# Kernel optimization log

Hardware: AMD Instinct MI355X
Metric: run time of the kernel (lower is better)

## Reference

```python
import jax, jax.numpy as jnp
import numpy as np

N_NODES = 100000


def gcn_conv(x, src, dst, W, b, n):
    # x: [N, F_in]; src/dst: [E+N] (self-loops already appended)
    h = x @ W  # [N, F_out]
    deg = jax.ops.segment_sum(jnp.ones_like(dst, dtype=h.dtype), dst, num_segments=n)
    dinv = jnp.where(deg > 0, jax.lax.rsqrt(deg), 0.0)
    norm = dinv[src] * dinv[dst]  # [E+N]
    msgs = h[src] * norm[:, None]  # gather + scale
    out = jax.ops.segment_sum(msgs, dst, num_segments=n)  # scatter-add at dst
    return out + b


def setup_inputs() -> dict:
    key = jax.random.key(0)
    k1, k2, k3, ke = jax.random.split(key, 4)
    d = 64
    x = jax.random.normal(k1, (N_NODES, d), dtype=jnp.float32)
    edge_index = jax.random.randint(ke, (2, 1000000), 0, N_NODES, dtype=jnp.int64)
    s = 1.0 / np.sqrt(d)
    W1 = jax.random.normal(k2, (d, d), dtype=jnp.float32) * s
    b1 = jnp.zeros((d,), dtype=jnp.float32)
    W2 = jax.random.normal(k3, (d, d), dtype=jnp.float32) * s
    b2 = jnp.zeros((d,), dtype=jnp.float32)
    return {"x": x, "edge_index": edge_index, "W1": W1, "b1": b1, "W2": W2, "b2": b2}


def reference(x, edge_index, W1, b1, W2, b2):
    n = x.shape[0]
    loops = jnp.arange(n, dtype=edge_index.dtype)
    src = jnp.concatenate([edge_index[0], loops])
    dst = jnp.concatenate([edge_index[1], loops])
    h = gcn_conv(x, src, dst, W1, b1, n)
    h = jax.nn.relu(h)
    out = gcn_conv(h, src, dst, W2, b2, n)
    return out
```

## Files before the change

### kernel.cpp

```cpp
#include <hip/hip_runtime.h>

#define F 64
#define NCH 64

typedef __attribute__((ext_vector_type(8))) short bf16x8;
typedef __attribute__((ext_vector_type(4))) float f32x4;

static __device__ __forceinline__ unsigned short f2bf(float f) {
    unsigned u = __float_as_uint(f);
    return (unsigned short)((u + 0x7fffu + ((u >> 16) & 1u)) >> 16);
}
static __device__ __forceinline__ float bflo(unsigned u) { return __uint_as_float(u << 16); }
static __device__ __forceinline__ float bfhi(unsigned u) { return __uint_as_float(u & 0xffff0000u); }

__global__ __launch_bounds__(256) void k_prep(const float* __restrict__ W1,
                                              const float* __restrict__ W2,
                                              unsigned short* __restrict__ W1t,
                                              unsigned short* __restrict__ W2t) {
    const float* W = blockIdx.x ? W2 : W1;
    unsigned short* Wt = blockIdx.x ? W2t : W1t;
    const int t = threadIdx.x;
#pragma unroll
    for (int i = 0; i < 16; ++i) {
        int e = t + i * 256;
        int n = e >> 6, k = e & 63;
        Wt[e] = f2bf(W[k * 64 + n]);
    }
}

__global__ __launch_bounds__(256) void k_hist(const int* __restrict__ dst,
                                              int* __restrict__ histM,
                                              int E, int chunk, int NB) {
    extern __shared__ int h[];
    const int t = threadIdx.x;
    for (int i = t; i < NB; i += 256) h[i] = 0;
    __syncthreads();
    const int lo = blockIdx.x * chunk;
    const int hi = min(E, lo + chunk);
    for (int e = lo + t; e < hi; e += 256) {
        atomicAdd(&h[dst[e] >> 8], 1);
    }
    __syncthreads();
    for (int i = t; i < NB; i += 256) histM[i * NCH + blockIdx.x] = h[i];
}

__global__ __launch_bounds__(256) void s_part(const int* __restrict__ v,
                                              int* __restrict__ part, int M) {
    __shared__ int sd[256];
    const int t = threadIdx.x;
    const int base = blockIdx.x * 1024 + t * 4;
    int4 d = *(const int4*)&v[base];
    sd[t] = d.x + d.y + d.z + d.w;
    __syncthreads();
    for (int off = 128; off > 0; off >>= 1) {
        if (t < off) sd[t] += sd[t + off];
        __syncthreads();
    }
    if (t == 0) part[blockIdx.x] = sd[0];
}

__global__ __launch_bounds__(256) void s_scanp(int* __restrict__ part, int nb) {
    __shared__ int sums[256];
    const int t = threadIdx.x;
    int s = (t < nb) ? part[t] : 0;
    sums[t] = s;
    __syncthreads();
    for (int off = 1; off < 256; off <<= 1) {
        int v = (t >= off) ? sums[t - off] : 0;
        __syncthreads();
        sums[t] += v;
        __syncthreads();
    }
    if (t < nb) part[t] = sums[t] - s;
}

__global__ __launch_bounds__(256) void s_emit(int* __restrict__ v,
                                              const int* __restrict__ part, int M) {
    __shared__ int sums[256];
    const int t = threadIdx.x;
    const int base = blockIdx.x * 1024 + t * 4;
    int4 d = *(const int4*)&v[base];
    int tot = d.x + d.y + d.z + d.w;
    sums[t] = tot;
    __syncthreads();
    for (int off = 1; off < 256; off <<= 1) {
        int x = (t >= off) ? sums[t - off] : 0;
        __syncthreads();
        sums[t] += x;
        __syncthreads();
    }
    int o0 = part[blockIdx.x] + sums[t] - tot;
    int4 o;
    o.x = o0; o.y = o0 + d.x; o.z = o.y + d.y; o.w = o.z + d.z;
    *(int4*)&v[base] = o;
}

__global__ __launch_bounds__(256) void k_scatter2(const int* __restrict__ src,
                                                  const int* __restrict__ dst,
                                                  const int* __restrict__ scanM,
                                                  int* __restrict__ ebuf,
                                                  int E, int chunk, int NB) {
    extern __shared__ int cur[];
    const int t = threadIdx.x;
    for (int i = t; i < NB; i += 256) cur[i] = scanM[i * NCH + blockIdx.x];
    __syncthreads();
    const int lo = blockIdx.x * chunk;
    const int hi = min(E, lo + chunk);
    for (int e = lo + t; e < hi; e += 256) {
        int s = src[e];
        int d = dst[e];
        int p = atomicAdd(&cur[d >> 8], 1);
        ebuf[p] = s | ((d & 255) << 17);
    }
}

__global__ __launch_bounds__(256) void k_csr(const int* __restrict__ ebuf,
                                             const int* __restrict__ scanM,
                                             int* __restrict__ rowptr,
                                             int* __restrict__ csr,
                                             float* __restrict__ dinv,
                                             int N, int E, int NB) {
    __shared__ int hist[256];
    __shared__ int scn[256];
    __shared__ int cur[256];
    const int t = threadIdx.x;
    const int bkt = blockIdx.x;
    const int beg = scanM[bkt * NCH];
    const int end = (bkt + 1 < NB) ? scanM[(bkt + 1) * NCH] : E;

    hist[t] = 0;
    __syncthreads();
    for (int e = beg + t; e < end; e += 256)
        atomicAdd(&hist[((unsigned)ebuf[e]) >> 17], 1);
    __syncthreads();

    scn[t] = hist[t];
    __syncthreads();
    for (int off = 1; off < 256; off <<= 1) {
        int v = (t >= off) ? scn[t - off] : 0;
        __syncthreads();
        scn[t] += v;
        __syncthreads();
    }

    {
        int excl = scn[t] - hist[t];
        int rp = beg + excl;
        int node = (bkt << 8) + t;
        cur[t] = rp;
        if (node < N) {
            rowptr[node] = rp;
            dinv[node] = rsqrtf((float)(hist[t] + 1));
        }
    }
    if (bkt == NB - 1 && t == 0) rowptr[N] = E;
    __syncthreads();

    for (int e = beg + t; e < end; e += 256) {
        int pk = ebuf[e];
        int p = atomicAdd(&cur[((unsigned)pk) >> 17], 1);
        csr[p] = pk & 0x1FFFF;
    }
}

__global__ __launch_bounds__(256) void k_gemm1(const float* __restrict__ X,
                                               const unsigned short* __restrict__ W1t,
                                               const float* __restrict__ dinv,
                                               unsigned short* __restrict__ hs, int N) {
    __shared__ unsigned short Wl[64 * 72];
    __shared__ unsigned short Xs[64 * 72];
    const int t = threadIdx.x;
    const int row0 = blockIdx.x * 64;

#pragma unroll
    for (int i = 0; i < 2; ++i) {
        int idx = t + i * 256;
        int n = idx >> 3, k = (idx & 7) * 8;
        *(uint4*)&Wl[n * 72 + k] = ((const uint4*)W1t)[idx];
    }
#pragma unroll
    for (int i = 0; i < 4; ++i) {
        int idx = t + i * 256;
        int r = idx >> 4, c = (idx & 15) * 4;
        int gr = row0 + r;
        float4 v = make_float4(0.f, 0.f, 0.f, 0.f);
        if (gr < N) v = *(const float4*)&X[(size_t)gr * F + c];
        unsigned p0 = (unsigned)f2bf(v.x) | ((unsigned)f2bf(v.y) << 16);
        unsigned p1 = (unsigned)f2bf(v.z) | ((unsigned)f2bf(v.w) << 16);
        *(uint2*)&Xs[r * 72 + c] = make_uint2(p0, p1);
    }
    __syncthreads();

    const int w    = t >> 6;
    const int lane = t & 63;
    const int l15  = lane & 15;
    const int quad = lane >> 4;

    bf16x8 bf[4][2];
#pragma unroll
    for (int ct = 0; ct < 4; ++ct)
#pragma unroll
        for (int kc = 0; kc < 2; ++kc)
            bf[ct][kc] = *(const bf16x8*)&Wl[(ct * 16 + l15) * 72 + kc * 32 + quad * 8];

    const int am = w * 16 + l15;
    bf16x8 af0 = *(const bf16x8*)&Xs[am * 72 + quad * 8];
    bf16x8 af1 = *(const bf16x8*)&Xs[am * 72 + 32 + quad * 8];

    f32x4 acc[4];
#pragma unroll
    for (int ct = 0; ct < 4; ++ct) {
        f32x4 z = {0.f, 0.f, 0.f, 0.f};
        z = __builtin_amdgcn_mfma_f32_16x16x32_bf16(af0, bf[ct][0], z, 0, 0, 0);
        z = __builtin_amdgcn_mfma_f32_16x16x32_bf16(af1, bf[ct][1], z, 0, 0, 0);
        acc[ct] = z;
    }

    float dv[4];
#pragma unroll
    for (int r = 0; r < 4; ++r) {
        int row = row0 + w * 16 + quad * 4 + r;
        dv[r] = (row < N) ? dinv[row] : 0.f;
    }
#pragma unroll
    for (int ct = 0; ct < 4; ++ct) {
#pragma unroll
        for (int r = 0; r < 4; ++r) {
            int row = row0 + w * 16 + quad * 4 + r;
            if (row < N)
                hs[(size_t)row * F + ct * 16 + l15] = f2bf(acc[ct][r] * dv[r]);
        }
    }
}

__global__ __launch_bounds__(512) void k_aggmm(const unsigned short* __restrict__ hs1,
                                               const int* __restrict__ rowptr,
                                               const int* __restrict__ csr,
                                               const unsigned short* __restrict__ W2t,
                                               const float* __restrict__ b1,
                                               unsigned short* __restrict__ hs2, int N) {
    __shared__ unsigned short Act[256 * 72];
    __shared__ unsigned short Wl[64 * 72];
    __shared__ float sdv[256];
    const int t = threadIdx.x;
    const int node0 = blockIdx.x << 8;

    if (t < 512) {
        int idx = t;
        int n = idx >> 3, k = (idx & 7) * 8;
        *(uint4*)&Wl[n * 72 + k] = ((const uint4*)W2t)[idx];
    }

    const int lane = t & 7;
    const int nsub = t >> 3;
    const uint4* hsb = (const uint4*)hs1;
    float4 bb0 = *(const float4*)&b1[lane * 8];
    float4 bb1 = *(const float4*)&b1[lane * 8 + 4];

#pragma unroll
    for (int it = 0; it < 4; ++it) {
        int local = it * 64 + nsub;
        int node = node0 + local;
        float sc = 0.f;
        unsigned p0 = 0, p1 = 0, p2 = 0, p3 = 0;
        if (node < N) {
            int beg = rowptr[node];
            int end = rowptr[node + 1];
            sc = rsqrtf((float)(end - beg + 1));
            float a0, a1, a2, a3, a4, a5, a6, a7;
            {
                uint4 u = hsb[(size_t)node * 8 + lane];
                a0 = bflo(u.x); a1 = bfhi(u.x);
                a2 = bflo(u.y); a3 = bfhi(u.y);
                a4 = bflo(u.z); a5 = bfhi(u.z);
                a6 = bflo(u.w); a7 = bfhi(u.w);
            }
            for (int base = beg; base < end; base += 16) {
                int i0 = base + lane;
                int i1 = base + 8 + lane;
                int x0 = (i0 < end) ? csr[i0] : 0;
                int x1 = (i1 < end) ? csr[i1] : 0;
                uint4 r[16];
#pragma unroll
                for (int k = 0; k < 8; ++k) {
                    int s = __shfl(x0, k, 8);
                    r[k] = hsb[(size_t)s * 8 + lane];
                }
#pragma unroll
                for (int k = 0; k < 8; ++k) {
                    int s = __shfl(x1, k, 8);
                    r[8 + k] = hsb[(size_t)s * 8 + lane];
                }
                int cnt = min(16, end - base);
#pragma unroll
                for (int k = 0; k < 16; ++k) {
                    if (k < cnt) {
                        uint4 u = r[k];
                        a0 += bflo(u.x); a1 += bfhi(u.x);
                        a2 += bflo(u.y); a3 += bfhi(u.y);
                        a4 += bflo(u.z); a5 += bfhi(u.z);
                        a6 += bflo(u.w); a7 += bfhi(u.w);
                    }
                }
            }
            float o0 = fmaxf(a0 * sc + bb0.x, 0.f), o1 = fmaxf(a1 * sc + bb0.y, 0.f);
            float o2 = fmaxf(a2 * sc + bb0.z, 0.f), o3 = fmaxf(a3 * sc + bb0.w, 0.f);
            float o4 = fmaxf(a4 * sc + bb1.x, 0.f), o5 = fmaxf(a5 * sc + bb1.y, 0.f);
            float o6 = fmaxf(a6 * sc + bb1.z, 0.f), o7 = fmaxf(a7 * sc + bb1.w, 0.f);
            p0 = (unsigned)f2bf(o0) | ((unsigned)f2bf(o1) << 16);
            p1 = (unsigned)f2bf(o2) | ((unsigned)f2bf(o3) << 16);
            p2 = (unsigned)f2bf(o4) | ((unsigned)f2bf(o5) << 16);
            p3 = (unsigned)f2bf(o6) | ((unsigned)f2bf(o7) << 16);
        }
        *(uint4*)&Act[local * 72 + lane * 8] = make_uint4(p0, p1, p2, p3);
        if (lane == 0) sdv[local] = sc;
    }
    __syncthreads();

    const int w    = t >> 6;
    const int l    = t & 63;
    const int l15  = l & 15;
    const int quad = l >> 4;

    bf16x8 bf[4][2];
#pragma unroll
    for (int nt = 0; nt < 4; ++nt)
#pragma unroll
        for (int kc = 0; kc < 2; ++kc)
            bf[nt][kc] = *(const bf16x8*)&Wl[(nt * 16 + l15) * 72 + kc * 32 + quad * 8];

#pragma unroll
    for (int mt = 0; mt < 2; ++mt) {
        int m0 = w * 32 + mt * 16;
        bf16x8 af0 = *(const bf16x8*)&Act[(m0 + l15) * 72 + quad * 8];
        bf16x8 af1 = *(const bf16x8*)&Act[(m0 + l15) * 72 + 32 + quad * 8];
#pragma unroll
        for (int nt = 0; nt < 4; ++nt) {
            f32x4 z = {0.f, 0.f, 0.f, 0.f};
            z = __builtin_amdgcn_mfma_f32_16x16x32_bf16(af0, bf[nt][0], z, 0, 0, 0);
            z = __builtin_amdgcn_mfma_f32_16x16x32_bf16(af1, bf[nt][1], z, 0, 0, 0);
#pragma unroll
            for (int r = 0; r < 4; ++r) {
                int row = m0 + quad * 4 + r;
                int node = node0 + row;
                if (node < N)
                    hs2[(size_t)node * F + nt * 16 + l15] = f2bf(z[r] * sdv[row]);
            }
        }
    }
}

__global__ __launch_bounds__(256) void k_agg(const unsigned short* __restrict__ hs,
                                             const int* __restrict__ rowptr,
                                             const int* __restrict__ csr,
                                             const float* __restrict__ dinv,
                                             const float* __restrict__ b,
                                             float* __restrict__ out, int N) {
    int gid = blockIdx.x * 256 + threadIdx.x;
    int node = gid >> 3;
    int lane = gid & 7;
    if (node >= N) return;
    int beg = rowptr[node];
    int end = rowptr[node + 1];
    const int q = lane * 8;
    const uint4* hsb = (const uint4*)hs;

    float acc0, acc1, acc2, acc3, acc4, acc5, acc6, acc7;
    {
        uint4 u = hsb[(size_t)node * 8 + lane];
        acc0 = bflo(u.x); acc1 = bfhi(u.x);
        acc2 = bflo(u.y); acc3 = bfhi(u.y);
        acc4 = bflo(u.z); acc5 = bfhi(u.z);
        acc6 = bflo(u.w); acc7 = bfhi(u.w);
    }
    for (int base = beg; base < end; base += 16) {
        int i0 = base + lane;
        int i1 = base + 8 + lane;
        int x0 = (i0 < end) ? csr[i0] : 0;
        int x1 = (i1 < end) ? csr[i1] : 0;
        uint4 r[16];
#pragma unroll
        for (int k = 0; k < 8; ++k) {
            int s = __shfl(x0, k, 8);
            r[k] = hsb[(size_t)s * 8 + lane];
        }
#pragma unroll
        for (int k = 0; k < 8; ++k) {
            int s = __shfl(x1, k, 8);
            r[8 + k] = hsb[(size_t)s * 8 + lane];
        }
        int cnt = min(16, end - base);
#pragma unroll
        for (int k = 0; k < 16; ++k) {
            if (k < cnt) {
                uint4 u = r[k];
                acc0 += bflo(u.x); acc1 += bfhi(u.x);
                acc2 += bflo(u.y); acc3 += bfhi(u.y);
                acc4 += bflo(u.z); acc5 += bfhi(u.z);
                acc6 += bflo(u.w); acc7 += bfhi(u.w);
            }
        }
    }

    float sc = dinv[node];
    float4 b0 = *(const float4*)&b[q];
    float4 b1 = *(const float4*)&b[q + 4];
    float4 o0 = make_float4(acc0 * sc + b0.x, acc1 * sc + b0.y,
                            acc2 * sc + b0.z, acc3 * sc + b0.w);
    float4 o1 = make_float4(acc4 * sc + b1.x, acc5 * sc + b1.y,
                            acc6 * sc + b1.z, acc7 * sc + b1.w);
    *(float4*)&out[(size_t)node * F + q] = o0;
    *(float4*)&out[(size_t)node * F + q + 4] = o1;
}

extern "C" void kernel_launch(void* const* d_in, const int* in_sizes, int n_in,
                              void* d_out, int out_size, void* d_ws, size_t ws_size,
                              hipStream_t stream) {
    const float* x  = (const float*)d_in[0];
    const int*   ei = (const int*)d_in[1];
    const float* W1 = (const float*)d_in[2];
    const float* b1 = (const float*)d_in[3];
    const float* W2 = (const float*)d_in[4];
    const float* b2 = (const float*)d_in[5];
    float* out = (float*)d_out;

    const int N = in_sizes[0] / F;
    const int E = in_sizes[1] / 2;
    const int* src = ei;
    const int* dst = ei + E;

    const int NB = (N + 255) >> 8;
    const int chunk = (E + NCH - 1) / NCH;
    const int M  = NB * NCH;
    const int Mp = ((M + 1023) / 1024) * 1024;
    const int nb2 = Mp / 1024;

    char* ws = (char*)d_ws;
    size_t a = 0;
    unsigned short* W1t = (unsigned short*)(ws + a); a += (4096 * 2 + 255) & ~(size_t)255;
    unsigned short* W2t = (unsigned short*)(ws + a); a += (4096 * 2 + 255) & ~(size_t)255;
    float* dinv   = (float*)(ws + a); a += ((size_t)N * 4 + 255) & ~(size_t)255;
    int*   part2  = (int*)(ws + a);   a += ((size_t)nb2 * 4 + 255) & ~(size_t)255;
    int*   rowptr = (int*)(ws + a);   a += ((size_t)(N + 1) * 4 + 255) & ~(size_t)255;
    int*   histM  = (int*)(ws + a);   a += ((size_t)Mp * 4 + 255) & ~(size_t)255;
    int*   ebuf   = (int*)(ws + a);   a += ((size_t)E * 4 + 255) & ~(size_t)255;
    int*   csr    = (int*)(ws + a);   a += ((size_t)E * 4 + 255) & ~(size_t)255;
    unsigned short* hs1 = (unsigned short*)(ws + a); a += ((size_t)N * F * 2 + 255) & ~(size_t)255;
    unsigned short* hs2 = (unsigned short*)(ws + a);

    const size_t ldsNB = (size_t)NB * 4;
    const int gGemm = (N + 63) / 64;
    const int gAgg  = (int)(((long long)N * 8 + 255) / 256);

    k_prep<<<2, 256, 0, stream>>>(W1, W2, W1t, W2t);
    hipMemsetAsync(histM, 0, (size_t)Mp * 4, stream);
    k_hist<<<NCH, 256, ldsNB, stream>>>(dst, histM, E, chunk, NB);
    s_part<<<nb2, 256, 0, stream>>>(histM, part2, Mp);
    s_scanp<<<1, 256, 0, stream>>>(part2, nb2);
    s_emit<<<nb2, 256, 0, stream>>>(histM, part2, Mp);
    k_scatter2<<<NCH, 256, ldsNB, stream>>>(src, dst, histM, ebuf, E, chunk, NB);
    k_csr<<<NB, 256, 0, stream>>>(ebuf, histM, rowptr, csr, dinv, N, E, NB);

    k_gemm1<<<gGemm, 256, 0, stream>>>(x, W1t, dinv, hs1, N);
    k_aggmm<<<NB, 512, 0, stream>>>(hs1, rowptr, csr, W2t, b1, hs2, N);
    k_agg<<<gAgg, 256, 0, stream>>>(hs2, rowptr, csr, dinv, b2, out, N);
}
```

Measured before the change: 198.3 us.

## Slice layer-2 features into column panels, merge weight prep into histogram, widen chunks

The second-layer hidden features are now written in four 16-column slices, each a contiguous panel. The final aggregation runs one block per slice, with two threads per node each gathering 32-byte rows, so every slice's working set is a quarter of the full table and is more likely to stay cache-resident. The weight conversion kernel is folded into the histogram launch as extra blocks, and the memset is dropped by bounding the scans at M. The number of histogram/scatter chunks goes from 64 to 256. In exchange, the new aggregation does fewer bytes per gather request and adds a cross-lane reduction, and the larger chunk count makes the count matrix and its scan four times bigger.

```diff
diff --git a/kernel.cpp b/kernel.cpp
--- a/kernel.cpp
+++ b/kernel.cpp
@@ -1,7 +1,7 @@
 #include <hip/hip_runtime.h>
 
 #define F 64
-#define NCH 64
+#define NCH 256
 
 typedef __attribute__((ext_vector_type(8))) short bf16x8;
 typedef __attribute__((ext_vector_type(4))) float f32x4;
@@ -13,26 +13,27 @@
 static __device__ __forceinline__ float bflo(unsigned u) { return __uint_as_float(u << 16); }
 static __device__ __forceinline__ float bfhi(unsigned u) { return __uint_as_float(u & 0xffff0000u); }
 
-__global__ __launch_bounds__(256) void k_prep(const float* __restrict__ W1,
-                                              const float* __restrict__ W2,
-                                              unsigned short* __restrict__ W1t,
-                                              unsigned short* __restrict__ W2t) {
-    const float* W = blockIdx.x ? W2 : W1;
-    unsigned short* Wt = blockIdx.x ? W2t : W1t;
-    const int t = threadIdx.x;
-#pragma unroll
-    for (int i = 0; i < 16; ++i) {
-        int e = t + i * 256;
-        int n = e >> 6, k = e & 63;
-        Wt[e] = f2bf(W[k * 64 + n]);
-    }
-}
-
-__global__ __launch_bounds__(256) void k_hist(const int* __restrict__ dst,
-                                              int* __restrict__ histM,
-                                              int E, int chunk, int NB) {
+__global__ __launch_bounds__(256) void k_histprep(const int* __restrict__ dst,
+                                                  int* __restrict__ histM,
+                                                  const float* __restrict__ W1,
+                                                  const float* __restrict__ W2,
+                                                  unsigned short* __restrict__ W1t,
+                                                  unsigned short* __restrict__ W2t,
+                                                  int E, int chunk, int NB) {
+    const int t = threadIdx.x;
+    if (blockIdx.x >= NCH) {
+        int which = blockIdx.x - NCH;
+        const float* W = which ? W2 : W1;
+        unsigned short* Wt = which ? W2t : W1t;
+#pragma unroll
+        for (int i = 0; i < 16; ++i) {
+            int e = t + i * 256;
+            int n = e >> 6, k = e & 63;
+            Wt[e] = f2bf(W[k * 64 + n]);
+        }
+        return;
+    }
     extern __shared__ int h[];
-    const int t = threadIdx.x;
     for (int i = t; i < NB; i += 256) h[i] = 0;
     __syncthreads();
     const int lo = blockIdx.x * chunk;
@@ -49,8 +50,15 @@
     __shared__ int sd[256];
     const int t = threadIdx.x;
     const int base = blockIdx.x * 1024 + t * 4;
-    int4 d = *(const int4*)&v[base];
-    sd[t] = d.x + d.y + d.z + d.w;
+    int s = 0;
+    if (base + 3 < M) {
+        int4 d = *(const int4*)&v[base];
+        s = d.x + d.y + d.z + d.w;
+    } else {
+#pragma unroll
+        for (int j = 0; j < 4; ++j) if (base + j < M) s += v[base + j];
+    }
+    sd[t] = s;
     __syncthreads();
     for (int off = 128; off > 0; off >>= 1) {
         if (t < off) sd[t] += sd[t + off];
@@ -79,8 +87,17 @@
     __shared__ int sums[256];
     const int t = threadIdx.x;
     const int base = blockIdx.x * 1024 + t * 4;
-    int4 d = *(const int4*)&v[base];
-    int tot = d.x + d.y + d.z + d.w;
+    int d0 = 0, d1 = 0, d2 = 0, d3 = 0;
+    if (base + 3 < M) {
+        int4 d = *(const int4*)&v[base];
+        d0 = d.x; d1 = d.y; d2 = d.z; d3 = d.w;
+    } else {
+        if (base + 0 < M) d0 = v[base + 0];
+        if (base + 1 < M) d1 = v[base + 1];
+        if (base + 2 < M) d2 = v[base + 2];
+        if (base + 3 < M) d3 = v[base + 3];
+    }
+    int tot = d0 + d1 + d2 + d3;
     sums[t] = tot;
     __syncthreads();
     for (int off = 1; off < 256; off <<= 1) {
@@ -90,9 +107,13 @@
         __syncthreads();
     }
     int o0 = part[blockIdx.x] + sums[t] - tot;
-    int4 o;
-    o.x = o0; o.y = o0 + d.x; o.z = o.y + d.y; o.w = o.z + d.z;
-    *(int4*)&v[base] = o;
+    int e0 = o0, e1 = o0 + d0, e2 = e1 + d1, e3 = e2 + d2;
+    if (base + 3 < M) {
+        *(int4*)&v[base] = make_int4(e0, e1, e2, e3);
+    } else {
+        int ee[4] = {e0, e1, e2, e3};
+        for (int j = 0; j < 4; ++j) if (base + j < M) v[base + j] = ee[j];
+    }
 }
 
 __global__ __launch_bounds__(256) void k_scatter2(const int* __restrict__ src,
@@ -245,7 +266,7 @@
     const int t = threadIdx.x;
     const int node0 = blockIdx.x << 8;
 
-    if (t < 512) {
+    {
         int idx = t;
         int n = idx >> 3, k = (idx & 7) * 8;
         *(uint4*)&Wl[n * 72 + k] = ((const uint4*)W2t)[idx];
@@ -344,73 +365,67 @@
                 int row = m0 + quad * 4 + r;
                 int node = node0 + row;
                 if (node < N)
-                    hs2[(size_t)node * F + nt * 16 + l15] = f2bf(z[r] * sdv[row]);
+                    hs2[((size_t)nt * N + node) * 16 + l15] = f2bf(z[r] * sdv[row]);
             }
         }
     }
 }
 
-__global__ __launch_bounds__(256) void k_agg(const unsigned short* __restrict__ hs,
-                                             const int* __restrict__ rowptr,
-                                             const int* __restrict__ csr,
-                                             const float* __restrict__ dinv,
-                                             const float* __restrict__ b,
-                                             float* __restrict__ out, int N) {
-    int gid = blockIdx.x * 256 + threadIdx.x;
-    int node = gid >> 3;
-    int lane = gid & 7;
+__global__ __launch_bounds__(256) void k_agg2(const unsigned short* __restrict__ hs2,
+                                              const int* __restrict__ rowptr,
+                                              const int* __restrict__ csr,
+                                              const float* __restrict__ dinv,
+                                              const float* __restrict__ b,
+                                              float* __restrict__ out, int N) {
+    const int slice = blockIdx.x & 3;
+    const int chunk = blockIdx.x >> 2;
+    const int t = threadIdx.x;
+    const int node = chunk * 128 + (t >> 1);
+    const int lane = t & 1;
     if (node >= N) return;
-    int beg = rowptr[node];
-    int end = rowptr[node + 1];
-    const int q = lane * 8;
-    const uint4* hsb = (const uint4*)hs;
-
-    float acc0, acc1, acc2, acc3, acc4, acc5, acc6, acc7;
-    {
-        uint4 u = hsb[(size_t)node * 8 + lane];
-        acc0 = bflo(u.x); acc1 = bfhi(u.x);
-        acc2 = bflo(u.y); acc3 = bfhi(u.y);
-        acc4 = bflo(u.z); acc5 = bfhi(u.z);
-        acc6 = bflo(u.w); acc7 = bfhi(u.w);
-    }
-    for (int base = beg; base < end; base += 16) {
-        int i0 = base + lane;
-        int i1 = base + 8 + lane;
-        int x0 = (i0 < end) ? csr[i0] : 0;
-        int x1 = (i1 < end) ? csr[i1] : 0;
-        uint4 r[16];
-#pragma unroll
-        for (int k = 0; k < 8; ++k) {
-            int s = __shfl(x0, k, 8);
-            r[k] = hsb[(size_t)s * 8 + lane];
-        }
-#pragma unroll
-        for (int k = 0; k < 8; ++k) {
-            int s = __shfl(x1, k, 8);
-            r[8 + k] = hsb[(size_t)s * 8 + lane];
-        }
-        int cnt = min(16, end - base);
-#pragma unroll
-        for (int k = 0; k < 16; ++k) {
-            if (k < cnt) {
-                uint4 u = r[k];
-                acc0 += bflo(u.x); acc1 += bfhi(u.x);
-                acc2 += bflo(u.y); acc3 += bfhi(u.y);
-                acc4 += bflo(u.z); acc5 += bfhi(u.z);
-                acc6 += bflo(u.w); acc7 += bfhi(u.w);
-            }
-        }
-    }
-
-    float sc = dinv[node];
-    float4 b0 = *(const float4*)&b[q];
-    float4 b1 = *(const float4*)&b[q + 4];
-    float4 o0 = make_float4(acc0 * sc + b0.x, acc1 * sc + b0.y,
-                            acc2 * sc + b0.z, acc3 * sc + b0.w);
-    float4 o1 = make_float4(acc4 * sc + b1.x, acc5 * sc + b1.y,
-                            acc6 * sc + b1.z, acc7 * sc + b1.w);
-    *(float4*)&out[(size_t)node * F + q] = o0;
-    *(float4*)&out[(size_t)node * F + q + 4] = o1;
+    const int beg = rowptr[node];
+    const int end = rowptr[node + 1];
+    const unsigned short* hp = hs2 + (size_t)slice * N * 16;
+
+    float a[16];
+#pragma unroll
+    for (int j = 0; j < 16; ++j) a[j] = 0.f;
+
+    for (int e = beg + lane; e < end; e += 2) {
+        int s = csr[e];
+        const uint4* p = (const uint4*)(hp + (size_t)s * 16);
+        uint4 u0 = p[0];
+        uint4 u1 = p[1];
+        a[0] += bflo(u0.x); a[1] += bfhi(u0.x);
+        a[2] += bflo(u0.y); a[3] += bfhi(u0.y);
+        a[4] += bflo(u0.z); a[5] += bfhi(u0.z);
+        a[6] += bflo(u0.w); a[7] += bfhi(u0.w);
+        a[8]  += bflo(u1.x); a[9]  += bfhi(u1.x);
+        a[10] += bflo(u1.y); a[11] += bfhi(u1.y);
+        a[12] += bflo(u1.z); a[13] += bfhi(u1.z);
+        a[14] += bflo(u1.w); a[15] += bfhi(u1.w);
+    }
+#pragma unroll
+    for (int j = 0; j < 16; ++j) a[j] += __shfl_xor(a[j], 1, 2);
+
+    const float sc = dinv[node];
+    const int j0 = lane * 8;
+    uint4 sv = *(const uint4*)(hp + (size_t)node * 16 + j0);
+    float s0 = bflo(sv.x), s1 = bfhi(sv.x), s2 = bflo(sv.y), s3 = bfhi(sv.y);
+    float s4 = bflo(sv.z), s5 = bfhi(sv.z), s6 = bflo(sv.w), s7 = bfhi(sv.w);
+    float4 bb0 = *(const float4*)&b[slice * 16 + j0];
+    float4 bb1 = *(const float4*)&b[slice * 16 + j0 + 4];
+    float4 o0 = make_float4((a[j0 + 0] + s0) * sc + bb0.x,
+                            (a[j0 + 1] + s1) * sc + bb0.y,
+                            (a[j0 + 2] + s2) * sc + bb0.z,
+                            (a[j0 + 3] + s3) * sc + bb0.w);
+    float4 o1 = make_float4((a[j0 + 4] + s4) * sc + bb1.x,
+                            (a[j0 + 5] + s5) * sc + bb1.y,
+                            (a[j0 + 6] + s6) * sc + bb1.z,
+                            (a[j0 + 7] + s7) * sc + bb1.w);
+    float* op = &out[(size_t)node * F + slice * 16 + j0];
+    *(float4*)op = o0;
+    *(float4*)(op + 4) = o1;
 }
 
 extern "C" void kernel_launch(void* const* d_in, const int* in_sizes, int n_in,
@@ -450,18 +465,16 @@
 
     const size_t ldsNB = (size_t)NB * 4;
     const int gGemm = (N + 63) / 64;
-    const int gAgg  = (int)(((long long)N * 8 + 255) / 256);
-
-    k_prep<<<2, 256, 0, stream>>>(W1, W2, W1t, W2t);
-    hipMemsetAsync(histM, 0, (size_t)Mp * 4, stream);
-    k_hist<<<NCH, 256, ldsNB, stream>>>(dst, histM, E, chunk, NB);
-    s_part<<<nb2, 256, 0, stream>>>(histM, part2, Mp);
+    const int gAgg2 = ((N + 127) / 128) * 4;
+
+    k_histprep<<<NCH + 2, 256, ldsNB, stream>>>(dst, histM, W1, W2, W1t, W2t, E, chunk, NB);
+    s_part<<<nb2, 256, 0, stream>>>(histM, part2, M);
     s_scanp<<<1, 256, 0, stream>>>(part2, nb2);
-    s_emit<<<nb2, 256, 0, stream>>>(histM, part2, Mp);
+    s_emit<<<nb2, 256, 0, stream>>>(histM, part2, M);
     k_scatter2<<<NCH, 256, ldsNB, stream>>>(src, dst, histM, ebuf, E, chunk, NB);
     k_csr<<<NB, 256, 0, stream>>>(ebuf, histM, rowptr, csr, dinv, N, E, NB);
 
     k_gemm1<<<gGemm, 256, 0, stream>>>(x, W1t, dinv, hs1, N);
     k_aggmm<<<NB, 512, 0, stream>>>(hs1, rowptr, csr, W2t, b1, hs2, N);
-    k_agg<<<gAgg, 256, 0, stream>>>(hs2, rowptr, csr, dinv, b2, out, N);
-}
+    k_agg2<<<gAgg2, 256, 0, stream>>>(hs2, rowptr, csr, dinv, b2, out, N);
+}
```

Result: faster. 190.6 us (-3.9%).
